# Kernel tuning notes

Measured on AMD Instinct MI355X. Metric: run time of the kernel, lower is better.

## Reference

```python
import jax, jax.numpy as jnp
import numpy as np

B, L, H = 2, 512, 768
W = 10          # span_width
K = 512         # topk pruned spans per doc
NL = 50         # num GCN labels
E = 2048        # edges per doc
NEG = -1e9


def setup_inputs() -> dict:
    key = jax.random.key(0)
    ks = jax.random.split(key, 16)
    embeddings = jax.random.normal(ks[0], (B, L, H), dtype=jnp.float32)
    src = jax.random.randint(ks[1], (B, E, 1), 0, L, dtype=jnp.int32)
    tgt = jax.random.randint(ks[2], (B, E, 1), 0, L, dtype=jnp.int32)
    lab = jax.random.randint(ks[3], (B, E, 1), 0, NL, dtype=jnp.int32)
    edges = jnp.concatenate([src, tgt, lab], axis=-1)  # [B,E,3]
    s = 0.02
    gcn_w = jax.random.normal(ks[4], (NL, H, H), dtype=jnp.float32) * s   # [label,out,in]
    gcn_b = jax.random.normal(ks[5], (NL, H), dtype=jnp.float32) * s
    attn_w = jax.random.normal(ks[6], (H,), dtype=jnp.float32) * s
    attn_b = jax.random.normal(ks[7], (1,), dtype=jnp.float32) * s
    m_w1 = jax.random.normal(ks[8], (3 * H, 3 * H), dtype=jnp.float32) * s
    m_b1 = jax.random.normal(ks[9], (3 * H,), dtype=jnp.float32) * s
    m_w2 = jax.random.normal(ks[10], (3 * H,), dtype=jnp.float32) * s
    m_b2 = jax.random.normal(ks[11], (1,), dtype=jnp.float32) * s
    ant_w = jax.random.normal(ks[12], (6 * H,), dtype=jnp.float32) * s
    ant_b = jax.random.normal(ks[13], (1,), dtype=jnp.float32) * s
    return dict(embeddings=embeddings, edges=edges, gcn_w=gcn_w, gcn_b=gcn_b,
                attn_w=attn_w, attn_b=attn_b, m_w1=m_w1, m_b1=m_b1,
                m_w2=m_w2, m_b2=m_b2, ant_w=ant_w, ant_b=ant_b)


def _forward(embeddings, edges, gcn_w, gcn_b, attn_w, attn_b,
             m_w1, m_b1, m_w2, m_b2, ant_w, ant_b):
    dt = embeddings.dtype
    src, tgt, lab = edges[..., 0], edges[..., 1], edges[..., 2]
    emask = (lab != -100) & (src < L) & (tgt < L)                       # [B,E]
    bidx = jnp.arange(B)[:, None]
    src_emb = embeddings[bidx, jnp.clip(src, 0, L - 1)]                 # [B,E,H]
    onehot = jax.nn.one_hot(jnp.clip(lab, 0, NL - 1), NL, dtype=dt)     # [B,E,NL]
    # per-label linear (loop over fixed small label set, not data dims)
    transformed = jnp.zeros_like(src_emb)
    for l in range(NL):
        transformed = transformed + onehot[..., l:l + 1] * (src_emb @ gcn_w[l].T + gcn_b[l])
    transformed = transformed * emask[..., None].astype(dt)
    flat_idx = (bidx * L + jnp.where(emask, tgt, 0)).reshape(-1)
    agg = jnp.zeros((B * L, H), dt).at[flat_idx].add(transformed.reshape(-1, H))
    deg = jnp.zeros((B * L,), dt).at[flat_idx].add(emask.reshape(-1).astype(dt))
    gcn_out = jax.nn.relu((agg / jnp.clip(deg, 1.0, None)[:, None]).reshape(B, L, H))
    emb = embeddings + gcn_out                                          # combine_strategy='add'

    # candidate spans: (s, s+w) for w in [0, W), valid iff s+w < L
    s_idx = jnp.repeat(jnp.arange(L), W)                                # [N]
    w_idx = jnp.tile(jnp.arange(W), L)                                  # [N]
    span_valid = (s_idx + w_idx) < L                                    # [N]
    pos = s_idx[:, None] + jnp.arange(W)[None, :]                       # [N,W]
    pos_mask = (jnp.arange(W)[None, :] <= w_idx[:, None]) & (pos < L)
    pos_c = jnp.clip(pos, 0, L - 1)

    attn_logits = emb @ attn_w + attn_b[0]                              # [B,L]
    g_logits = jnp.where(pos_mask[None], attn_logits[:, pos_c], NEG)    # [B,N,W]
    attn = jax.nn.softmax(g_logits, axis=-1)
    g_emb = emb[:, pos_c]                                               # [B,N,W,H]
    pooled = jnp.einsum('bnw,bnwh->bnh', attn, g_emb)
    start_emb = emb[:, s_idx]
    end_emb = emb[:, jnp.clip(s_idx + w_idx, 0, L - 1)]
    span_rep = jnp.concatenate([start_emb, end_emb, pooled], axis=-1)   # [B,N,3H]

    hid = jax.nn.relu(span_rep @ m_w1.T + m_b1)
    m_scores = hid @ m_w2 + m_b2[0]                                     # [B,N]
    m_scores = jnp.where(span_valid[None], m_scores, NEG)

    topk_scores, topk_idx = jax.lax.top_k(m_scores, K)                  # [B,K]
    pruned = jnp.take_along_axis(span_rep, topk_idx[..., None], axis=1) # [B,K,3H]

    # antecedent scorer on cat([rep_j, rep_i]) decomposed: score[i,j] = Wa.rep_j + Wb.rep_i + b
    Wa, Wb = ant_w[:3 * H], ant_w[3 * H:]
    sa = pruned @ Wa                                                    # [B,K]
    sb = pruned @ Wb
    ant_scores = sb[:, :, None] + sa[:, None, :] + ant_b[0]             # [B,K,K]
    return ant_scores


def reference(embeddings, edges, gcn_w, gcn_b, attn_w, attn_b,
              m_w1, m_b1, m_w2, m_b2, ant_w, ant_b):
    return _forward(embeddings, edges, gcn_w, gcn_b, attn_w, attn_b,
                    m_w1, m_b1, m_w2, m_b2, ant_w, ant_b)
```

## Files before the change

### kernel.cpp

```cpp
#include <hip/hip_runtime.h>
#include <math.h>

#define BB 2
#define LL 512
#define HH 768
#define WSP 10
#define KTOP 512
#define NLAB 50
#define EE 2048
#define NSPAN 5120
#define H3 2304
#define NEGVD -1000000000.0

__device__ inline double atomAddD(double* a, double v){
  return __hip_atomic_fetch_add(a, v, __ATOMIC_RELAXED, __HIP_MEMORY_SCOPE_AGENT);
}

__global__ void bucket_kernel(const int* __restrict__ edges, int* __restrict__ offsets,
                              int* __restrict__ sorted, float* __restrict__ deg){
  __shared__ int cnt[NLAB];
  __shared__ int pos[NLAB];
  int t = threadIdx.x;
  if (t < NLAB) cnt[t] = 0;
  __syncthreads();
  for (int i = t; i < BB*EE; i += 256){
    int src = edges[i*3+0], tgt = edges[i*3+1], lab = edges[i*3+2];
    bool ok = (lab != -100) && (src < LL) && (tgt < LL);
    if (ok){
      int lc = min(max(lab,0), NLAB-1);
      atomicAdd(&cnt[lc], 1);
      int b = i / EE;
      int tg = min(max(tgt,0), LL-1);
      atomicAdd(&deg[b*LL + tg], 1.0f);
    }
  }
  __syncthreads();
  if (t == 0){
    int s = 0;
    for (int l = 0; l < NLAB; l++){ offsets[l] = s; pos[l] = s; s += cnt[l]; }
    offsets[NLAB] = s;
  }
  __syncthreads();
  for (int i = t; i < BB*EE; i += 256){
    int src = edges[i*3+0], tgt = edges[i*3+1], lab = edges[i*3+2];
    bool ok = (lab != -100) && (src < LL) && (tgt < LL);
    if (ok){
      int lc = min(max(lab,0), NLAB-1);
      int p = atomicAdd(&pos[lc], 1);
      sorted[p] = i;
    }
  }
}

__global__ __launch_bounds__(256) void gcn_gemm(const float* __restrict__ embeddings,
    const int* __restrict__ edges, const float* __restrict__ gcn_w,
    const float* __restrict__ gcn_b, const int* __restrict__ offsets,
    const int* __restrict__ sorted, double* __restrict__ agg_d){
  int l = blockIdx.y;
  int off = offsets[l];
  int cnt = offsets[l+1] - off;
  int m0 = blockIdx.z * 128;
  if (m0 >= cnt) return;
  int n0 = blockIdx.x * 128;
  __shared__ float As[32][132];
  __shared__ float Bs[32][132];
  __shared__ int rbase[128];
  __shared__ int rtgt[128];
  int t = threadIdx.x;
  if (t < 128){
    int m = m0 + t;
    if (m < cnt){
      int id = sorted[off + m];
      int b = id / EE;
      int src = edges[id*3+0]; src = min(max(src,0), LL-1);
      int tgt = edges[id*3+1]; tgt = min(max(tgt,0), LL-1);
      rbase[t] = (b*LL + src) * HH;
      rtgt[t]  = b*LL + tgt;
    } else { rbase[t] = -1; rtgt[t] = -1; }
  }
  double acc[8][8];
  #pragma unroll
  for (int i=0;i<8;i++)
    #pragma unroll
    for (int j=0;j<8;j++) acc[i][j]=0.0;
  int lr = t >> 3;
  int lk = (t & 7) * 4;
  int tx = t & 15, ty = t >> 4;
  const float* Wl = gcn_w + (size_t)l * HH * HH;
  for (int k0 = 0; k0 < HH; k0 += 32){
    __syncthreads();
    #pragma unroll
    for (int r = 0; r < 4; r++){
      int m = lr + r*32;
      float4 va = make_float4(0.f,0.f,0.f,0.f);
      int rb = rbase[m];
      if (rb >= 0) va = *(const float4*)&embeddings[rb + k0 + lk];
      As[lk+0][m]=va.x; As[lk+1][m]=va.y; As[lk+2][m]=va.z; As[lk+3][m]=va.w;
      float4 vb = *(const float4*)&Wl[(size_t)(n0+m)*HH + k0 + lk];
      Bs[lk+0][m]=vb.x; Bs[lk+1][m]=vb.y; Bs[lk+2][m]=vb.z; Bs[lk+3][m]=vb.w;
    }
    __syncthreads();
    #pragma unroll 4
    for (int k = 0; k < 32; k++){
      float4 a0 = *(const float4*)&As[k][ty*8];
      float4 a1 = *(const float4*)&As[k][ty*8+4];
      float4 bq0 = *(const float4*)&Bs[k][tx*4];
      float4 bq1 = *(const float4*)&Bs[k][64+tx*4];
      double av[8] = {(double)a0.x,(double)a0.y,(double)a0.z,(double)a0.w,
                      (double)a1.x,(double)a1.y,(double)a1.z,(double)a1.w};
      double bv[8] = {(double)bq0.x,(double)bq0.y,(double)bq0.z,(double)bq0.w,
                      (double)bq1.x,(double)bq1.y,(double)bq1.z,(double)bq1.w};
      #pragma unroll
      for (int i=0;i<8;i++)
        #pragma unroll
        for (int j=0;j<8;j++) acc[i][j] = fma(av[i], bv[j], acc[i][j]);
    }
  }
  #pragma unroll
  for (int i=0;i<8;i++){
    int m = ty*8 + i;
    int dst = rtgt[m];
    if (dst < 0) continue;
    #pragma unroll
    for (int j=0;j<8;j++){
      int h = n0 + ((j<4)? tx*4+j : 64+tx*4+(j-4));
      atomAddD(&agg_d[(size_t)dst*HH + h], acc[i][j] + (double)gcn_b[l*HH + h]);
    }
  }
}

__global__ __launch_bounds__(256) void emb_kernel(const float* __restrict__ embeddings,
    const double* __restrict__ agg_d, const float* __restrict__ deg,
    const float* __restrict__ attn_w, const float* __restrict__ attn_b,
    float* __restrict__ emb, double* __restrict__ logits_d){
  int bid = blockIdx.x;
  int t = threadIdx.x;
  double d = (double)fmaxf(deg[bid], 1.0f);
  size_t base = (size_t)bid * HH;
  double part = 0.0;
  #pragma unroll
  for (int c = 0; c < 3; c++){
    int h = t + c*256;
    double g = agg_d[base+h] / d;
    if (g < 0.0) g = 0.0;
    float v = embeddings[base+h] + (float)g;
    emb[base+h] = v;
    part += (double)v * (double)attn_w[h];
  }
  #pragma unroll
  for (int dl = 1; dl < 64; dl <<= 1) part += __shfl_xor(part, dl);
  __shared__ double wred[4];
  if ((t & 63) == 0) wred[t >> 6] = part;
  __syncthreads();
  if (t == 0) logits_d[bid] = wred[0]+wred[1]+wred[2]+wred[3] + (double)attn_b[0];
}

__global__ __launch_bounds__(256) void span_kernel(const float* __restrict__ emb,
    const double* __restrict__ logits_d, float* __restrict__ span_rep){
  int bid = blockIdx.x;
  int b = bid / LL, s = bid % LL;
  int t = threadIdx.x;
  __shared__ float rows[WSP][HH];
  __shared__ double aw[WSP][WSP];
  __shared__ double lg[WSP];
  for (int idx = t; idx < WSP*HH; idx += 256){
    int j = idx / HH, h = idx % HH;
    int r = min(s + j, LL-1);
    rows[j][h] = emb[((size_t)b*LL + r)*HH + h];
  }
  if (t < WSP) lg[t] = logits_d[b*LL + min(s + t, LL-1)];
  __syncthreads();
  if (t < WSP){
    int w = t;
    double mx = -1.0e300;
    for (int j = 0; j <= w; j++) if (s + j < LL) mx = fmax(mx, lg[j]);
    double sum = 0.0;
    for (int j = 0; j < WSP; j++){
      double e = 0.0;
      if (j <= w && s + j < LL) e = exp(lg[j] - mx);
      aw[w][j] = e; sum += e;
    }
    double inv = 1.0 / sum;
    for (int j = 0; j < WSP; j++) aw[w][j] *= inv;
  }
  __syncthreads();
  for (int w = 0; w < WSP; w++){
    size_t obase = ((size_t)b*NSPAN + s*WSP + w) * H3;
    int erow = min(w, LL-1-s);
    #pragma unroll
    for (int c = 0; c < 3; c++){
      int h = t + c*256;
      double pooled = 0.0;
      for (int j = 0; j <= w; j++) pooled = fma(aw[w][j], (double)rows[j][h], pooled);
      span_rep[obase + h]        = rows[0][h];
      span_rep[obase + HH + h]   = rows[erow][h];
      span_rep[obase + 2*HH + h] = (float)pooled;
    }
  }
}

__global__ __launch_bounds__(256) void mlp_gemm(const float* __restrict__ sr,
    const float* __restrict__ w1, const float* __restrict__ b1,
    const float* __restrict__ w2, double* __restrict__ msc){
  int bid = blockIdx.x;
  int b2 = (bid & 7) * 180 + (bid >> 3);
  int mb = b2 / 18, nb = b2 % 18;
  int m0 = mb * 128, n0 = nb * 128;
  __shared__ float As[32][132];
  __shared__ float Bs[32][132];
  int t = threadIdx.x;
  double acc[8][8];
  #pragma unroll
  for (int i=0;i<8;i++)
    #pragma unroll
    for (int j=0;j<8;j++) acc[i][j]=0.0;
  int lr = t >> 3;
  int lk = (t & 7) * 4;
  int tx = t & 15, ty = t >> 4;
  for (int k0 = 0; k0 < H3; k0 += 32){
    __syncthreads();
    #pragma unroll
    for (int r = 0; r < 4; r++){
      int m = lr + r*32;
      float4 va = *(const float4*)&sr[(size_t)(m0+m)*H3 + k0 + lk];
      As[lk+0][m]=va.x; As[lk+1][m]=va.y; As[lk+2][m]=va.z; As[lk+3][m]=va.w;
      float4 vb = *(const float4*)&w1[(size_t)(n0+m)*H3 + k0 + lk];
      Bs[lk+0][m]=vb.x; Bs[lk+1][m]=vb.y; Bs[lk+2][m]=vb.z; Bs[lk+3][m]=vb.w;
    }
    __syncthreads();
    #pragma unroll 4
    for (int k = 0; k < 32; k++){
      float4 a0 = *(const float4*)&As[k][ty*8];
      float4 a1 = *(const float4*)&As[k][ty*8+4];
      float4 bq0 = *(const float4*)&Bs[k][tx*4];
      float4 bq1 = *(const float4*)&Bs[k][64+tx*4];
      double av[8] = {(double)a0.x,(double)a0.y,(double)a0.z,(double)a0.w,
                      (double)a1.x,(double)a1.y,(double)a1.z,(double)a1.w};
      double bv[8] = {(double)bq0.x,(double)bq0.y,(double)bq0.z,(double)bq0.w,
                      (double)bq1.x,(double)bq1.y,(double)bq1.z,(double)bq1.w};
      #pragma unroll
      for (int i=0;i<8;i++)
        #pragma unroll
        for (int j=0;j<8;j++) acc[i][j] = fma(av[i], bv[j], acc[i][j]);
    }
  }
  double bbd[8], wwd[8];
  #pragma unroll
  for (int j=0;j<8;j++){
    int h = n0 + ((j<4)? tx*4+j : 64+tx*4+(j-4));
    bbd[j] = (double)b1[h]; wwd[j] = (double)w2[h];
  }
  #pragma unroll
  for (int i=0;i<8;i++){
    double p = 0.0;
    #pragma unroll
    for (int j=0;j<8;j++){
      double hv = acc[i][j] + bbd[j];
      p += (hv > 0.0 ? hv : 0.0) * wwd[j];
    }
    p += __shfl_xor(p, 1); p += __shfl_xor(p, 2);
    p += __shfl_xor(p, 4); p += __shfl_xor(p, 8);
    if (tx == 0) atomAddD(&msc[m0 + ty*8 + i], p);
  }
}

__global__ __launch_bounds__(1024) void topk_kernel(const double* __restrict__ msc,
    const float* __restrict__ m_b2, int* __restrict__ tidx){
  int b = blockIdx.x;
  int t = threadIdx.x;
  __shared__ double sc[NSPAN];
  __shared__ double wv[16];
  __shared__ int wi[16];
  __shared__ int bwin;
  double b2d = (double)m_b2[0];
  #pragma unroll
  for (int i = 0; i < 5; i++){
    int n = t + i*1024;
    int s = n / WSP, w = n % WSP;
    double v = (s + w < LL) ? (msc[b*NSPAN + n] + b2d) : NEGVD;
    sc[n] = v;
  }
  __syncthreads();
  double lv = sc[t]; int li = t;
  #pragma unroll
  for (int i = 1; i < 5; i++){
    int n = t + i*1024;
    double v = sc[n];
    if (v > lv){ lv = v; li = n; }
  }
  for (int k = 0; k < KTOP; k++){
    double v = lv; int idx = li;
    #pragma unroll
    for (int m = 1; m < 64; m <<= 1){
      double ov = __shfl_xor(v, m);
      int oi = __shfl_xor(idx, m);
      if (ov > v || (ov == v && oi < idx)){ v = ov; idx = oi; }
    }
    if ((t & 63) == 0){ wv[t >> 6] = v; wi[t >> 6] = idx; }
    __syncthreads();
    if (t < 16){
      double v2 = wv[t]; int i2 = wi[t];
      #pragma unroll
      for (int m = 1; m < 16; m <<= 1){
        double ov = __shfl_xor(v2, m);
        int oi = __shfl_xor(i2, m);
        if (ov > v2 || (ov == v2 && oi < i2)){ v2 = ov; i2 = oi; }
      }
      if (t == 0){ tidx[b*KTOP + k] = i2; bwin = i2; }
    }
    __syncthreads();
    int n = bwin;
    if ((n & 1023) == t){
      sc[n] = -1.0e308;
      lv = sc[t]; li = t;
      #pragma unroll
      for (int i = 1; i < 5; i++){
        int nn = t + i*1024;
        double vv = sc[nn];
        if (vv > lv){ lv = vv; li = nn; }
      }
    }
    __syncthreads();
  }
}

__global__ __launch_bounds__(256) void prune_kernel(const float* __restrict__ span_rep,
    const int* __restrict__ tidx, const float* __restrict__ ant_w,
    double* __restrict__ sa, double* __restrict__ sb){
  int bid = blockIdx.x;
  int b = bid / KTOP;
  int t = threadIdx.x;
  int idx = tidx[bid];
  const float* row = span_rep + ((size_t)b*NSPAN + idx) * H3;
  double pa = 0.0, pb = 0.0;
  for (int h = t; h < H3; h += 256){
    double x = (double)row[h];
    pa = fma(x, (double)ant_w[h], pa);
    pb = fma(x, (double)ant_w[H3 + h], pb);
  }
  #pragma unroll
  for (int dl = 1; dl < 64; dl <<= 1){ pa += __shfl_xor(pa, dl); pb += __shfl_xor(pb, dl); }
  __shared__ double ra[4], rb[4];
  if ((t & 63) == 0){ ra[t>>6] = pa; rb[t>>6] = pb; }
  __syncthreads();
  if (t == 0){
    sa[bid] = ra[0]+ra[1]+ra[2]+ra[3];
    sb[bid] = rb[0]+rb[1]+rb[2]+rb[3];
  }
}

__global__ void final_kernel(const double* __restrict__ sa, const double* __restrict__ sb,
                             const float* __restrict__ ant_b, float* __restrict__ out){
  int o = blockIdx.x*256 + threadIdx.x;
  if (o >= BB*KTOP*KTOP) return;
  int j = o & (KTOP-1);
  int i = (o >> 9) & (KTOP-1);
  int b = o >> 18;
  out[o] = (float)(sb[b*KTOP + i] + sa[b*KTOP + j] + (double)ant_b[0]);
}

extern "C" void kernel_launch(void* const* d_in, const int* in_sizes, int n_in,
                              void* d_out, int out_size, void* d_ws, size_t ws_size,
                              hipStream_t stream) {
  const float* embeddings = (const float*)d_in[0];
  const int*   edges      = (const int*)  d_in[1];
  const float* gcn_w      = (const float*)d_in[2];
  const float* gcn_b      = (const float*)d_in[3];
  const float* attn_w     = (const float*)d_in[4];
  const float* attn_b     = (const float*)d_in[5];
  const float* m_w1       = (const float*)d_in[6];
  const float* m_b1       = (const float*)d_in[7];
  const float* m_w2       = (const float*)d_in[8];
  const float* m_b2       = (const float*)d_in[9];
  const float* ant_w      = (const float*)d_in[10];
  const float* ant_b      = (const float*)d_in[11];
  float* out = (float*)d_out;

  double* agg_d    = (double*)d_ws;
  double* msc_d    = agg_d + (size_t)BB*LL*HH;
  float*  deg      = (float*)(msc_d + BB*NSPAN);
  double* logits_d = (double*)(deg + BB*LL);
  double* sa_d     = logits_d + BB*LL;
  double* sb_d     = sa_d + BB*KTOP;
  float*  emb      = (float*)(sb_d + BB*KTOP);
  float*  span_rep = emb + (size_t)BB*LL*HH;
  int*    tki      = (int*)(span_rep + (size_t)BB*NSPAN*H3);
  int*    offs     = tki + BB*KTOP;
  int*    sorted   = offs + 64;

  hipMemsetAsync(agg_d, 0,
                 (size_t)BB*LL*HH*8 + (size_t)BB*NSPAN*8 + (size_t)BB*LL*4, stream);

  bucket_kernel<<<1, 256, 0, stream>>>(edges, offs, sorted, deg);
  gcn_gemm<<<dim3(HH/128, NLAB, 4), 256, 0, stream>>>(embeddings, edges, gcn_w, gcn_b,
                                                      offs, sorted, agg_d);
  emb_kernel<<<BB*LL, 256, 0, stream>>>(embeddings, agg_d, deg, attn_w, attn_b, emb, logits_d);
  span_kernel<<<BB*LL, 256, 0, stream>>>(emb, logits_d, span_rep);
  mlp_gemm<<<1440, 256, 0, stream>>>(span_rep, m_w1, m_b1, m_w2, msc_d);
  topk_kernel<<<BB, 1024, 0, stream>>>(msc_d, m_b2, tki);
  prune_kernel<<<BB*KTOP, 256, 0, stream>>>(span_rep, tki, ant_w, sa_d, sb_d);
  final_kernel<<<(BB*KTOP*KTOP+255)/256, 256, 0, stream>>>(sa_d, sb_d, ant_b, out);
}
```

Baseline: 3.780 ms.

## Score spans in fp32, then rescore top candidates in fp64 before top-k

```diff
diff --git a/kernel.cpp b/kernel.cpp
--- a/kernel.cpp
+++ b/kernel.cpp
@@ -11,6 +11,8 @@
 #define NSPAN 5120
 #define H3 2304
 #define NEGVD -1000000000.0
+#define CAND_CAP 1280
+#define CAND_TILES 10
 
 __device__ inline double atomAddD(double* a, double v){
   return __hip_atomic_fetch_add(a, v, __ATOMIC_RELAXED, __HIP_MEMORY_SCOPE_AGENT);
@@ -199,9 +201,9 @@
   }
 }
 
-__global__ __launch_bounds__(256) void mlp_gemm(const float* __restrict__ sr,
+__global__ __launch_bounds__(256) void mlp_gemm_f32(const float* __restrict__ sr,
     const float* __restrict__ w1, const float* __restrict__ b1,
-    const float* __restrict__ w2, double* __restrict__ msc){
+    const float* __restrict__ w2, float* __restrict__ mscf){
   int bid = blockIdx.x;
   int b2 = (bid & 7) * 180 + (bid >> 3);
   int mb = b2 / 18, nb = b2 % 18;
@@ -209,6 +211,134 @@
   __shared__ float As[32][132];
   __shared__ float Bs[32][132];
   int t = threadIdx.x;
+  float acc[8][8];
+  #pragma unroll
+  for (int i=0;i<8;i++)
+    #pragma unroll
+    for (int j=0;j<8;j++) acc[i][j]=0.f;
+  int lr = t >> 3;
+  int lk = (t & 7) * 4;
+  int tx = t & 15, ty = t >> 4;
+  for (int k0 = 0; k0 < H3; k0 += 32){
+    __syncthreads();
+    #pragma unroll
+    for (int r = 0; r < 4; r++){
+      int m = lr + r*32;
+      float4 va = *(const float4*)&sr[(size_t)(m0+m)*H3 + k0 + lk];
+      As[lk+0][m]=va.x; As[lk+1][m]=va.y; As[lk+2][m]=va.z; As[lk+3][m]=va.w;
+      float4 vb = *(const float4*)&w1[(size_t)(n0+m)*H3 + k0 + lk];
+      Bs[lk+0][m]=vb.x; Bs[lk+1][m]=vb.y; Bs[lk+2][m]=vb.z; Bs[lk+3][m]=vb.w;
+    }
+    __syncthreads();
+    #pragma unroll 8
+    for (int k = 0; k < 32; k++){
+      float4 a0 = *(const float4*)&As[k][ty*8];
+      float4 a1 = *(const float4*)&As[k][ty*8+4];
+      float4 bq0 = *(const float4*)&Bs[k][tx*4];
+      float4 bq1 = *(const float4*)&Bs[k][64+tx*4];
+      float av[8] = {a0.x,a0.y,a0.z,a0.w,a1.x,a1.y,a1.z,a1.w};
+      float bv[8] = {bq0.x,bq0.y,bq0.z,bq0.w,bq1.x,bq1.y,bq1.z,bq1.w};
+      #pragma unroll
+      for (int i=0;i<8;i++)
+        #pragma unroll
+        for (int j=0;j<8;j++) acc[i][j] = fmaf(av[i], bv[j], acc[i][j]);
+    }
+  }
+  float bb[8], wwv[8];
+  #pragma unroll
+  for (int j=0;j<8;j++){
+    int h = n0 + ((j<4)? tx*4+j : 64+tx*4+(j-4));
+    bb[j] = b1[h]; wwv[j] = w2[h];
+  }
+  #pragma unroll
+  for (int i=0;i<8;i++){
+    float p = 0.f;
+    #pragma unroll
+    for (int j=0;j<8;j++) p += fmaxf(acc[i][j] + bb[j], 0.f) * wwv[j];
+    p += __shfl_xor(p, 1); p += __shfl_xor(p, 2);
+    p += __shfl_xor(p, 4); p += __shfl_xor(p, 8);
+    if (tx == 0) atomicAdd(&mscf[m0 + ty*8 + i], p);
+  }
+}
+
+__global__ __launch_bounds__(1024) void select_kernel(const float* __restrict__ mscf,
+    int* __restrict__ cand_idx, int* __restrict__ iscand){
+  int b = blockIdx.x, t = threadIdx.x;
+  __shared__ unsigned keys[NSPAN];
+  __shared__ int hist[4096];
+  __shared__ int sh_bkt, sh_need, sh_cnt;
+  #pragma unroll
+  for (int i = 0; i < 5; i++){
+    int n = t + i*1024;
+    int s = n / WSP, w = n % WSP;
+    float v = (s + w < LL) ? mscf[b*NSPAN + n] : -3.4e38f;
+    unsigned u = __float_as_uint(v);
+    keys[n] = (u & 0x80000000u) ? ~u : (u | 0x80000000u);
+  }
+  if (t == 0) sh_cnt = 0;
+  __syncthreads();
+  unsigned prefix = 0u, pmask = 0u;
+  int need = 1024;
+  const int shifts[3] = {22, 12, 0};
+  const int nbk[3] = {1024, 1024, 4096};
+  for (int lvl = 0; lvl < 3; lvl++){
+    int B = nbk[lvl], sh = shifts[lvl];
+    for (int j = t; j < B; j += 1024) hist[j] = 0;
+    __syncthreads();
+    #pragma unroll
+    for (int i = 0; i < 5; i++){
+      unsigned k = keys[t + i*1024];
+      if ((k & pmask) == prefix) atomicAdd(&hist[(k >> sh) & (B-1)], 1);
+    }
+    __syncthreads();
+    if (t == 0){
+      int cum = 0, bkt = 0, nd = need;
+      for (int j = B-1; j >= 0; j--){
+        if (cum + hist[j] >= need){ bkt = j; nd = need - cum; break; }
+        cum += hist[j];
+      }
+      sh_bkt = bkt; sh_need = nd;
+    }
+    __syncthreads();
+    prefix |= ((unsigned)sh_bkt) << sh;
+    pmask  |= ((unsigned)(B-1)) << sh;
+    need = sh_need;
+    __syncthreads();
+  }
+  unsigned T = prefix;
+  #pragma unroll
+  for (int i = 0; i < 5; i++){
+    int n = t + i*1024;
+    if (keys[n] >= T){
+      int p = atomicAdd(&sh_cnt, 1);
+      if (p < CAND_CAP){ cand_idx[b*CAND_CAP + p] = n; iscand[b*NSPAN + n] = 1; }
+      else iscand[b*NSPAN + n] = 0;
+    } else iscand[b*NSPAN + n] = 0;
+  }
+  __syncthreads();
+  int cnt = min(sh_cnt, CAND_CAP);
+  for (int p = t; p < CAND_CAP; p += 1024)
+    if (p >= cnt) cand_idx[b*CAND_CAP + p] = -1;
+}
+
+__global__ __launch_bounds__(256) void mlp_cand_f64(const float* __restrict__ sr,
+    const float* __restrict__ w1, const float* __restrict__ b1,
+    const float* __restrict__ w2, const int* __restrict__ cand_idx,
+    double* __restrict__ msc){
+  int nb = blockIdx.x;
+  int mt = blockIdx.y;
+  int b  = blockIdx.z;
+  int n0 = nb * 128;
+  __shared__ float As[32][132];
+  __shared__ float Bs[32][132];
+  __shared__ int rbase[128];
+  __shared__ int rowix[128];
+  int t = threadIdx.x;
+  if (t < 128){
+    int row = cand_idx[b*CAND_CAP + mt*128 + t];
+    rowix[t] = row;
+    rbase[t] = (row >= 0) ? (b*NSPAN + row) * H3 : -1;
+  }
   double acc[8][8];
   #pragma unroll
   for (int i=0;i<8;i++)
@@ -222,7 +352,9 @@
     #pragma unroll
     for (int r = 0; r < 4; r++){
       int m = lr + r*32;
-      float4 va = *(const float4*)&sr[(size_t)(m0+m)*H3 + k0 + lk];
+      float4 va = make_float4(0.f,0.f,0.f,0.f);
+      int rb = rbase[m];
+      if (rb >= 0) va = *(const float4*)&sr[(size_t)rb + k0 + lk];
       As[lk+0][m]=va.x; As[lk+1][m]=va.y; As[lk+2][m]=va.z; As[lk+3][m]=va.w;
       float4 vb = *(const float4*)&w1[(size_t)(n0+m)*H3 + k0 + lk];
       Bs[lk+0][m]=vb.x; Bs[lk+1][m]=vb.y; Bs[lk+2][m]=vb.z; Bs[lk+3][m]=vb.w;
@@ -252,6 +384,7 @@
   }
   #pragma unroll
   for (int i=0;i<8;i++){
+    int row = rowix[ty*8 + i];
     double p = 0.0;
     #pragma unroll
     for (int j=0;j<8;j++){
@@ -260,12 +393,13 @@
     }
     p += __shfl_xor(p, 1); p += __shfl_xor(p, 2);
     p += __shfl_xor(p, 4); p += __shfl_xor(p, 8);
-    if (tx == 0) atomAddD(&msc[m0 + ty*8 + i], p);
+    if (tx == 0 && row >= 0) atomAddD(&msc[b*NSPAN + row], p);
   }
 }
 
 __global__ __launch_bounds__(1024) void topk_kernel(const double* __restrict__ msc,
-    const float* __restrict__ m_b2, int* __restrict__ tidx){
+    const float* __restrict__ m_b2, const int* __restrict__ iscand,
+    int* __restrict__ tidx){
   int b = blockIdx.x;
   int t = threadIdx.x;
   __shared__ double sc[NSPAN];
@@ -277,7 +411,7 @@
   for (int i = 0; i < 5; i++){
     int n = t + i*1024;
     int s = n / WSP, w = n % WSP;
-    double v = (s + w < LL) ? (msc[b*NSPAN + n] + b2d) : NEGVD;
+    double v = (s + w < LL && iscand[b*NSPAN + n]) ? (msc[b*NSPAN + n] + b2d) : NEGVD;
     sc[n] = v;
   }
   __syncthreads();
@@ -378,7 +512,8 @@
 
   double* agg_d    = (double*)d_ws;
   double* msc_d    = agg_d + (size_t)BB*LL*HH;
-  float*  deg      = (float*)(msc_d + BB*NSPAN);
+  float*  msc_f    = (float*)(msc_d + BB*NSPAN);
+  float*  deg      = msc_f + BB*NSPAN;
   double* logits_d = (double*)(deg + BB*LL);
   double* sa_d     = logits_d + BB*LL;
   double* sb_d     = sa_d + BB*KTOP;
@@ -387,17 +522,23 @@
   int*    tki      = (int*)(span_rep + (size_t)BB*NSPAN*H3);
   int*    offs     = tki + BB*KTOP;
   int*    sorted   = offs + 64;
+  int*    cand_idx = sorted + 4096;
+  int*    iscand   = cand_idx + BB*CAND_CAP;
 
   hipMemsetAsync(agg_d, 0,
-                 (size_t)BB*LL*HH*8 + (size_t)BB*NSPAN*8 + (size_t)BB*LL*4, stream);
+                 (size_t)BB*LL*HH*8 + (size_t)BB*NSPAN*8 + (size_t)BB*NSPAN*4
+                 + (size_t)BB*LL*4, stream);
 
   bucket_kernel<<<1, 256, 0, stream>>>(edges, offs, sorted, deg);
   gcn_gemm<<<dim3(HH/128, NLAB, 4), 256, 0, stream>>>(embeddings, edges, gcn_w, gcn_b,
                                                       offs, sorted, agg_d);
   emb_kernel<<<BB*LL, 256, 0, stream>>>(embeddings, agg_d, deg, attn_w, attn_b, emb, logits_d);
   span_kernel<<<BB*LL, 256, 0, stream>>>(emb, logits_d, span_rep);
-  mlp_gemm<<<1440, 256, 0, stream>>>(span_rep, m_w1, m_b1, m_w2, msc_d);
-  topk_kernel<<<BB, 1024, 0, stream>>>(msc_d, m_b2, tki);
+  mlp_gemm_f32<<<1440, 256, 0, stream>>>(span_rep, m_w1, m_b1, m_w2, msc_f);
+  select_kernel<<<BB, 1024, 0, stream>>>(msc_f, cand_idx, iscand);
+  mlp_cand_f64<<<dim3(18, CAND_TILES, BB), 256, 0, stream>>>(span_rep, m_w1, m_b1, m_w2,
+                                                             cand_idx, msc_d);
+  topk_kernel<<<BB, 1024, 0, stream>>>(msc_d, m_b2, iscand, tki);
   prune_kernel<<<BB*KTOP, 256, 0, stream>>>(span_rep, tki, ant_w, sa_d, sb_d);
   final_kernel<<<(BB*KTOP*KTOP+255)/256, 256, 0, stream>>>(sa_d, sb_d, ant_b, out);
 }
```

Measured after the change: 3.823 ms. Within noise of the previous version (+1.1%).
